# Performance work log

Hardware: AMD Instinct MI355X
Metric: run time of the kernel (lower is better)

Reference implementation:

```python
import jax, jax.numpy as jnp
import numpy as np


def setup_inputs() -> dict:
    key = jax.random.key(0)
    k1, k2, k3, k4 = jax.random.split(key, 4)
    B, I, P, F = 4096, 1024, 512, 2048
    x = jax.random.normal(k1, (B, I), dtype=jnp.float32)
    # params initialized like torch.rand(...)*2-1 (uniform in [-1,1])
    features = jax.random.uniform(k2, (F, I), dtype=jnp.float32, minval=-1.0, maxval=1.0)
    prototypes = jax.random.uniform(k3, (P, I), dtype=jnp.float32, minval=-1.0, maxval=1.0)
    # scalars: torch inits to zeros; use small nonzero values so output/grads are informative
    abt = jax.random.normal(k4, (3,), dtype=jnp.float32) * 0.1
    alpha = abt[0:1]
    beta = abt[1:2]
    theta = abt[2:3]
    return {"x": x, "features": features, "prototypes": prototypes,
            "alpha": alpha, "beta": beta, "theta": theta}


def reference(x, features, prototypes, alpha, beta, theta):
    # x: [b, i], features: [f, i], prototypes: [p, i]
    # Original einsums broadcast over p but the projection is p-independent:
    xf = x @ features.T            # [b, f]
    pf = prototypes @ features.T   # [p, f]
    x_pres = jax.nn.relu(xf)       # [b, f]
    p_pres = jax.nn.relu(pf)       # [p, f]
    # common[b,p]       = sum_f xf*pf*relu(xf)*relu(pf)
    # x_distinct[b,p]   = sum_f xf*relu(xf)*(1-relu(pf))
    # p_distinct[b,p]   = sum_f pf*relu(pf)*(1-relu(xf))
    a = xf * x_pres                # [b, f]
    c = pf * p_pres                # [p, f]
    common = a @ c.T                                   # [b, p]
    x_distinctive = a @ (1.0 - p_pres).T               # [b, p]
    p_distinctive = (1.0 - x_pres) @ c.T               # [b, p]
    return theta * common - alpha * x_distinctive - beta * p_distinctive
```

## Files before the change

### kernel.cpp

```cpp
#include <hip/hip_runtime.h>
#include <cstdint>

typedef __attribute__((ext_vector_type(8))) short bf16x8;
typedef __attribute__((ext_vector_type(16))) float f32x16;
typedef __attribute__((ext_vector_type(4))) float f4;
typedef __attribute__((ext_vector_type(8))) unsigned short u16x8;
typedef unsigned short u16;


__device__ __forceinline__ u16 f2bf(float f) {
  uint32_t u = __builtin_bit_cast(uint32_t, f);
  u += 0x7fffu + ((u >> 16) & 1u);
  return (u16)(u >> 16);
}

__device__ __forceinline__ void async_cp16(const void* g, void* l) {
  __builtin_amdgcn_global_load_lds(
      (const __attribute__((address_space(1))) uint32_t*)g,
      (__attribute__((address_space(3))) uint32_t*)l, 16, 0, 0);
}

__global__ __launch_bounds__(256) void cast3(
    const float* __restrict__ x, const float* __restrict__ f,
    const float* __restrict__ p, u16* __restrict__ dst,
    int n1, int n2, int n3) {
  int i = (blockIdx.x * 256 + threadIdx.x) * 8;
  const float* src;
  int local;
  if (i < n1) { src = x; local = i; }
  else if (i < n1 + n2) { src = f; local = i - n1; }
  else if (i < n1 + n2 + n3) { src = p; local = i - n1 - n2; }
  else return;
  f4 a = *(const f4*)(src + local);
  f4 b = *(const f4*)(src + local + 4);
  u16x8 o;
  o[0] = f2bf(a.x); o[1] = f2bf(a.y); o[2] = f2bf(a.z); o[3] = f2bf(a.w);
  o[4] = f2bf(b.x); o[5] = f2bf(b.y); o[6] = f2bf(b.z); o[7] = f2bf(b.w);
  *(u16x8*)(dst + i) = o;
}

__device__ __forceinline__ void mainloop(
    const u16* __restrict__ A, const u16* __restrict__ B, int K,
    int kbeg, int kend, int tid, u16* lds, f32x16 (&acc)[2]) {
  constexpr int TM = 128, TN = 64, BK = 64;
  const int lane = tid & 63;
  const int wave = tid >> 6;
  const int wrow = wave >> 1, wcol = wave & 1;

  for (int k0 = kbeg; k0 < kend; k0 += BK) {
    #pragma unroll
    for (int it = 0; it < TM / 32; ++it) {
      int c = it * 256 + tid;
      int row = c >> 3, pc = c & 7;
      int gc = pc ^ (row & 7);
      async_cp16(A + (size_t)row * K + (k0 + gc * 8),
                 &lds[(it * 256 + wave * 64) * 8]);
    }
    #pragma unroll
    for (int it = 0; it < TN / 32; ++it) {
      int c = it * 256 + tid;
      int row = c >> 3, pc = c & 7;
      int gc = pc ^ (row & 7);
      async_cp16(B + (size_t)row * K + (k0 + gc * 8),
                 &lds[TM * BK + (it * 256 + wave * 64) * 8]);
    }
    __syncthreads();

    #pragma unroll
    for (int s = 0; s < 4; ++s) {
      const int h = s * 2 + (lane >> 5);
      const int rb = wcol * 32 + (lane & 31);
      bf16x8 bfr = *(const bf16x8*)&lds[TM * BK + (rb * 8 + (h ^ (rb & 7))) * 8];
      #pragma unroll
      for (int i = 0; i < 2; ++i) {
        const int ra = wrow * 64 + i * 32 + (lane & 31);
        bf16x8 afr = *(const bf16x8*)&lds[(ra * 8 + (h ^ (ra & 7))) * 8];
        acc[i] = __builtin_amdgcn_mfma_f32_32x32x16_bf16(afr, bfr, acc[i], 0, 0, 0);
      }
    }
    __syncthreads();
  }
}


__global__ __launch_bounds__(256) void gemm12(
    const u16* __restrict__ xb, const u16* __restrict__ pb,
    const u16* __restrict__ fb, u16* __restrict__ Acat, u16* __restrict__ Bcat,
    const float* __restrict__ alpha, const float* __restrict__ beta,
    const float* __restrict__ theta) {
  constexpr int TM = 128, TN = 64, K = 1024, N = 2048;
  constexpr int TSTRIDE = 72;
  __shared__ u16 lds[(TM + TN) * 64];

  const int tid = threadIdx.x;
  const int lane = tid & 63;
  const int wave = tid >> 6;
  const int wrow = wave >> 1, wcol = wave & 1;
  const int bm_all = blockIdx.x * TM;
  const int bn = blockIdx.y * TN;
  const bool is_x = bm_all < 4096;
  const u16* A = is_x ? xb + (size_t)bm_all * K : pb + (size_t)(bm_all - 4096) * K;
  const u16* B = fb + (size_t)bn * K;

  f32x16 acc[2] = {};
  mainloop(A, B, K, 0, K, tid, lds, acc);

  float th = 0.f, al = 0.f, be = 0.f;
  if (!is_x) { th = theta[0]; al = alpha[0]; be = beta[0]; }
  u16* dst = is_x ? Acat : Bcat;
  const int rowbase = is_x ? bm_all : bm_all - 4096;
  const int cl = wcol * 32 + (lane & 31);
  const int rquad = 4 * (lane >> 5);

  #pragma unroll
  for (int half = 0; half < 2; ++half) {
    __syncthreads();
    #pragma unroll
    for (int i = 0; i < 2; ++i) {
      #pragma unroll
      for (int r = 0; r < 16; ++r) {
        const int rl = wrow * 64 + i * 32 + (r & 3) + 8 * (r >> 2) + rquad;
        float v = acc[i][r];
        float pres = v > 0.f ? v : 0.f;
        float o;
        if (is_x) o = half == 0 ? v * pres : 1.f - pres;
        else {
          float cc = v * pres;
          o = half == 0 ? th * cc - al * (1.f - pres) : -be * cc;
        }
        lds[rl * TSTRIDE + cl] = f2bf(o);
      }
    }
    __syncthreads();
    #pragma unroll
    for (int v = 0; v < 4; ++v) {
      const int rl = v * 32 + (tid >> 3);
      const int c8 = (tid & 7) * 8;
      u16x8 vec = *(const u16x8*)&lds[rl * TSTRIDE + c8];
      *(u16x8*)&dst[(size_t)(rowbase + rl) * (2 * N) + bn + c8 + half * N] = vec;
    }
  }
}

__global__ __launch_bounds__(256) void gemm3(
    const u16* __restrict__ Acat, const u16* __restrict__ Bcat,
    float* __restrict__ part) {
  constexpr int TM = 128, TN = 64, K = 4096, KSPLIT = 4;
  __shared__ u16 lds[(TM + TN) * 64];

  const int tid = threadIdx.x;
  const int bm = blockIdx.x * TM;
  const int bn = blockIdx.y * TN;
  const int kbeg = blockIdx.z * (K / KSPLIT);
  const int kend = kbeg + (K / KSPLIT);

  f32x16 acc[2] = {};
  mainloop(Acat + (size_t)bm * K, Bcat + (size_t)bn * K, K, kbeg, kend,
           tid, lds, acc);

  const size_t pbase =
      ((size_t)blockIdx.z * 256 + blockIdx.y * 32 + blockIdx.x) * 8192;
  #pragma unroll
  for (int i = 0; i < 2; ++i)
    #pragma unroll
    for (int q = 0; q < 4; ++q) {
      f4 v = {acc[i][q * 4 + 0], acc[i][q * 4 + 1],
              acc[i][q * 4 + 2], acc[i][q * 4 + 3]};
      *(f4*)&part[pbase + (i * 4 + q) * 1024 + tid * 4] = v;
    }
}

__global__ __launch_bounds__(256) void reduce4(
    const float* __restrict__ part, float* __restrict__ out) {
  constexpr int N = 512;
  const int tid = threadIdx.x;
  const int lane = tid & 63;
  const int wave = tid >> 6;
  const int wrow = wave >> 1, wcol = wave & 1;
  const int tileId = blockIdx.x;
  const int bm = (tileId & 31) * 128;
  const int bn = (tileId >> 5) * 64;
  const int gc = bn + wcol * 32 + (lane & 31);
  const int rquad = 4 * (lane >> 5);

  #pragma unroll
  for (int s = 0; s < 8; ++s) {
    f4 v = {0.f, 0.f, 0.f, 0.f};
    #pragma unroll
    for (int z = 0; z < 4; ++z)
      v += *(const f4*)&part[((size_t)z * 256 + tileId) * 8192 + s * 1024 + tid * 4];
    const int i = s >> 2, q = s & 3;
    const int gr0 = bm + wrow * 64 + i * 32 + 8 * q + rquad;
    out[(size_t)(gr0 + 0) * N + gc] = v.x;
    out[(size_t)(gr0 + 1) * N + gc] = v.y;
    out[(size_t)(gr0 + 2) * N + gc] = v.z;
    out[(size_t)(gr0 + 3) * N + gc] = v.w;
  }
}

extern "C" void kernel_launch(void* const* d_in, const int* in_sizes, int n_in,
                              void* d_out, int out_size, void* d_ws, size_t ws_size,
                              hipStream_t stream) {
  const float* x     = (const float*)d_in[0];
  const float* feat  = (const float*)d_in[1];
  const float* proto = (const float*)d_in[2];
  const float* alpha = (const float*)d_in[3];
  const float* beta  = (const float*)d_in[4];
  const float* theta = (const float*)d_in[5];
  float* out = (float*)d_out;

  constexpr int Bb = 4096, Ii = 1024, Pp = 512, Ff = 2048;

  char* ws = (char*)d_ws;
  u16* xb    = (u16*)ws;
  u16* fb    = xb + (size_t)Bb * Ii;
  u16* pb    = fb + (size_t)Ff * Ii;
  float* part = (float*)ws;
  size_t r0 = (size_t)4 * 256 * 8192 * 4;
  u16* Acat = (u16*)(ws + r0);
  u16* Bcat = Acat + (size_t)Bb * 2 * Ff;

  const int n1 = Bb * Ii, n2 = Ff * Ii, n3 = Pp * Ii;
  cast3<<<((n1 + n2 + n3) / 8 + 255) / 256, 256, 0, stream>>>(
      x, feat, proto, xb, n1, n2, n3);

  gemm12<<<dim3(36, 32), 256, 0, stream>>>(xb, pb, fb, Acat, Bcat, alpha, beta, theta);

  gemm3<<<dim3(Bb / 128, Pp / 64, 4), 256, 0, stream>>>(Acat, Bcat, part);

  reduce4<<<256, 256, 0, stream>>>(part, out);
}
```

Before: 148.4 us.

## Enlarge gemm3 tile, double split-K, store bf16 partials

The final GEMM now uses a 256x64 tile, with each wave computing a 2x2 block of MFMA tiles so fragments are reused, and split-K rises from 4 to 8. Partial sums are written as bf16 instead of fp32, which keeps the partial buffer the same size despite twice as many splits. The reduce kernel sums eight bf16 partials per output. This cuts LDS fragment loads per MFMA and partial-sum traffic, but rounding partial sums to bf16 adds accuracy error.

```diff
diff --git a/kernel.cpp b/kernel.cpp
--- a/kernel.cpp
+++ b/kernel.cpp
@@ -12,6 +12,10 @@
   uint32_t u = __builtin_bit_cast(uint32_t, f);
   u += 0x7fffu + ((u >> 16) & 1u);
   return (u16)(u >> 16);
+}
+
+__device__ __forceinline__ float bf2f(u16 h) {
+  return __builtin_bit_cast(float, (uint32_t)h << 16);
 }
 
 __device__ __forceinline__ void async_cp16(const void* g, void* l) {
@@ -144,57 +148,110 @@
 
 __global__ __launch_bounds__(256) void gemm3(
     const u16* __restrict__ Acat, const u16* __restrict__ Bcat,
-    float* __restrict__ part) {
-  constexpr int TM = 128, TN = 64, K = 4096, KSPLIT = 4;
+    u16* __restrict__ part) {
+  constexpr int TM = 256, TN = 64, K = 4096, KSPLIT = 8;
   __shared__ u16 lds[(TM + TN) * 64];
 
   const int tid = threadIdx.x;
+  const int lane = tid & 63;
+  const int wave = tid >> 6;
   const int bm = blockIdx.x * TM;
   const int bn = blockIdx.y * TN;
   const int kbeg = blockIdx.z * (K / KSPLIT);
   const int kend = kbeg + (K / KSPLIT);
-
-  f32x16 acc[2] = {};
-  mainloop(Acat + (size_t)bm * K, Bcat + (size_t)bn * K, K, kbeg, kend,
-           tid, lds, acc);
+  const u16* A = Acat + (size_t)bm * K;
+  const u16* B = Bcat + (size_t)bn * K;
+
+  f32x16 acc[2][2] = {};
+  for (int k0 = kbeg; k0 < kend; k0 += 64) {
+    #pragma unroll
+    for (int it = 0; it < TM / 32; ++it) {
+      int c = it * 256 + tid;
+      int row = c >> 3, pc = c & 7;
+      int gc = pc ^ (row & 7);
+      async_cp16(A + (size_t)row * K + (k0 + gc * 8),
+                 &lds[(it * 256 + wave * 64) * 8]);
+    }
+    #pragma unroll
+    for (int it = 0; it < TN / 32; ++it) {
+      int c = it * 256 + tid;
+      int row = c >> 3, pc = c & 7;
+      int gc = pc ^ (row & 7);
+      async_cp16(B + (size_t)row * K + (k0 + gc * 8),
+                 &lds[TM * 64 + (it * 256 + wave * 64) * 8]);
+    }
+    __syncthreads();
+
+    #pragma unroll
+    for (int s = 0; s < 4; ++s) {
+      const int h = s * 2 + (lane >> 5);
+      bf16x8 afr[2], bfr[2];
+      #pragma unroll
+      for (int i = 0; i < 2; ++i) {
+        const int ra = wave * 64 + i * 32 + (lane & 31);
+        afr[i] = *(const bf16x8*)&lds[(ra * 8 + (h ^ (ra & 7))) * 8];
+      }
+      #pragma unroll
+      for (int j = 0; j < 2; ++j) {
+        const int rb = j * 32 + (lane & 31);
+        bfr[j] = *(const bf16x8*)&lds[TM * 64 + (rb * 8 + (h ^ (rb & 7))) * 8];
+      }
+      #pragma unroll
+      for (int i = 0; i < 2; ++i)
+        #pragma unroll
+        for (int j = 0; j < 2; ++j)
+          acc[i][j] = __builtin_amdgcn_mfma_f32_32x32x16_bf16(afr[i], bfr[j],
+                                                              acc[i][j], 0, 0, 0);
+    }
+    __syncthreads();
+  }
 
   const size_t pbase =
-      ((size_t)blockIdx.z * 256 + blockIdx.y * 32 + blockIdx.x) * 8192;
+      ((size_t)blockIdx.z * 128 + blockIdx.y * 16 + blockIdx.x) * 16384;
   #pragma unroll
   for (int i = 0; i < 2; ++i)
     #pragma unroll
-    for (int q = 0; q < 4; ++q) {
-      f4 v = {acc[i][q * 4 + 0], acc[i][q * 4 + 1],
-              acc[i][q * 4 + 2], acc[i][q * 4 + 3]};
-      *(f4*)&part[pbase + (i * 4 + q) * 1024 + tid * 4] = v;
-    }
-}
-
-__global__ __launch_bounds__(256) void reduce4(
-    const float* __restrict__ part, float* __restrict__ out) {
+    for (int j = 0; j < 2; ++j)
+      #pragma unroll
+      for (int h = 0; h < 2; ++h) {
+        u16x8 o;
+        #pragma unroll
+        for (int e = 0; e < 8; ++e) o[e] = f2bf(acc[i][j][h * 8 + e]);
+        *(u16x8*)&part[pbase + ((i * 2 + j) * 2 + h) * 2048 + tid * 8] = o;
+      }
+}
+
+__global__ __launch_bounds__(256) void reduce8(
+    const u16* __restrict__ part, float* __restrict__ out) {
   constexpr int N = 512;
   const int tid = threadIdx.x;
   const int lane = tid & 63;
-  const int wave = tid >> 6;
-  const int wrow = wave >> 1, wcol = wave & 1;
-  const int tileId = blockIdx.x;
-  const int bm = (tileId & 31) * 128;
-  const int bn = (tileId >> 5) * 64;
-  const int gc = bn + wcol * 32 + (lane & 31);
+  const int w = tid >> 6;
+  const int tileId = blockIdx.x >> 1;
+  const int s0 = (blockIdx.x & 1) * 4;
+  const int bm = (tileId & 15) * 256;
+  const int bn = (tileId >> 4) * 64;
   const int rquad = 4 * (lane >> 5);
 
   #pragma unroll
-  for (int s = 0; s < 8; ++s) {
-    f4 v = {0.f, 0.f, 0.f, 0.f};
-    #pragma unroll
-    for (int z = 0; z < 4; ++z)
-      v += *(const f4*)&part[((size_t)z * 256 + tileId) * 8192 + s * 1024 + tid * 4];
-    const int i = s >> 2, q = s & 3;
-    const int gr0 = bm + wrow * 64 + i * 32 + 8 * q + rquad;
-    out[(size_t)(gr0 + 0) * N + gc] = v.x;
-    out[(size_t)(gr0 + 1) * N + gc] = v.y;
-    out[(size_t)(gr0 + 2) * N + gc] = v.z;
-    out[(size_t)(gr0 + 3) * N + gc] = v.w;
+  for (int t = 0; t < 4; ++t) {
+    const int s = s0 + t;
+    float v[8] = {};
+    #pragma unroll
+    for (int z = 0; z < 8; ++z) {
+      u16x8 u = *(const u16x8*)&part[((size_t)z * 128 + tileId) * 16384 +
+                                     s * 2048 + tid * 8];
+      #pragma unroll
+      for (int e = 0; e < 8; ++e) v[e] += bf2f(u[e]);
+    }
+    const int i = s >> 2, j = (s >> 1) & 1, h = s & 1;
+    const int gc = bn + j * 32 + (lane & 31);
+    const int grb = bm + w * 64 + i * 32 + rquad;
+    #pragma unroll
+    for (int e = 0; e < 8; ++e) {
+      const int reg = h * 8 + e;
+      out[(size_t)(grb + (reg & 3) + 8 * (reg >> 2)) * N + gc] = v[e];
+    }
   }
 }
 
@@ -212,11 +269,11 @@
   constexpr int Bb = 4096, Ii = 1024, Pp = 512, Ff = 2048;
 
   char* ws = (char*)d_ws;
-  u16* xb    = (u16*)ws;
-  u16* fb    = xb + (size_t)Bb * Ii;
-  u16* pb    = fb + (size_t)Ff * Ii;
-  float* part = (float*)ws;
-  size_t r0 = (size_t)4 * 256 * 8192 * 4;
+  u16* xb   = (u16*)ws;
+  u16* fb   = xb + (size_t)Bb * Ii;
+  u16* pb   = fb + (size_t)Ff * Ii;
+  u16* part = (u16*)ws;
+  size_t r0 = (size_t)8 * 128 * 16384 * 2;
   u16* Acat = (u16*)(ws + r0);
   u16* Bcat = Acat + (size_t)Bb * 2 * Ff;
 
@@ -226,7 +283,7 @@
 
   gemm12<<<dim3(36, 32), 256, 0, stream>>>(xb, pb, fb, Acat, Bcat, alpha, beta, theta);
 
-  gemm3<<<dim3(Bb / 128, Pp / 64, 4), 256, 0, stream>>>(Acat, Bcat, part);
-
-  reduce4<<<256, 256, 0, stream>>>(part, out);
-}
+  gemm3<<<dim3(Bb / 256, Pp / 64, 8), 256, 0, stream>>>(Acat, Bcat, part);
+
+  reduce8<<<256, 256, 0, stream>>>(part, out);
+}
```

Result: no change. 149.2 us (+0.5%).
